# Kernel optimization log

Measured on AMD Instinct MI355X. Metric: run time of the kernel, lower is better.

Reference implementation:

```python
import jax, jax.numpy as jnp
import numpy as np

NEG_SLOPE = 0.01  # torch F.leaky_relu default
N_USER = 100000
N_ITEM = 100000
N_EDGE = 640000
D = 128
N_LAYERS = 3  # 1 input + num_hidden_layers(1) + 1 output layer


def setup_inputs() -> dict:
    key = jax.random.key(0)
    ks = jax.random.split(key, 10)
    scale = 1.0 / np.sqrt(D)
    return {
        "h_user": jax.random.normal(ks[0], (N_USER, D), dtype=jnp.float32),
        "h_item": jax.random.normal(ks[1], (N_ITEM, D), dtype=jnp.float32),
        # W[layer, etype] : etype 0 = user-follows->user, 1 = user-clicks->item, 2 = item-clicked_by->user
        "W": jax.random.normal(ks[2], (N_LAYERS, 3, D, D), dtype=jnp.float32) * scale,
        "b": jnp.zeros((N_LAYERS, 3, D), dtype=jnp.float32),
        "follows_src": jax.random.randint(ks[3], (N_EDGE,), 0, N_USER, dtype=jnp.int32),
        "follows_dst": jax.random.randint(ks[4], (N_EDGE,), 0, N_USER, dtype=jnp.int32),
        "clicks_src": jax.random.randint(ks[5], (N_EDGE,), 0, N_USER, dtype=jnp.int32),
        "clicks_dst": jax.random.randint(ks[6], (N_EDGE,), 0, N_ITEM, dtype=jnp.int32),
        "cb_src": jax.random.randint(ks[7], (N_EDGE,), 0, N_ITEM, dtype=jnp.int32),
        "cb_dst": jax.random.randint(ks[8], (N_EDGE,), 0, N_USER, dtype=jnp.int32),
    }


def _etype_conv(h_src, W, b, src, dst, n_dst):
    """Per-etype Linear on src nodes, copy_u gather, mean-aggregate at dst."""
    Wh = h_src @ W + b                     # [N_src, D] dense transform (once per node)
    msg = Wh[src]                          # [E, D] gather
    s = jax.ops.segment_sum(msg, dst, num_segments=n_dst)
    cnt = jax.ops.segment_sum(jnp.ones((src.shape[0],), dtype=Wh.dtype), dst, num_segments=n_dst)
    return s / jnp.maximum(cnt, 1.0)[:, None]  # mean; isolated nodes -> 0


def _rgcn_forward(h_user, h_item, W, b, follows_src, follows_dst,
                  clicks_src, clicks_dst, cb_src, cb_dst):
    hu, hi = h_user, h_item
    for l in range(N_LAYERS):
        # per-etype mean aggregation, then cross-etype 'sum' (DGL multi_update_all)
        agg_u = (_etype_conv(hu, W[l, 0], b[l, 0], follows_src, follows_dst, N_USER)
                 + _etype_conv(hi, W[l, 2], b[l, 2], cb_src, cb_dst, N_USER))
        agg_i = _etype_conv(hu, W[l, 1], b[l, 1], clicks_src, clicks_dst, N_ITEM)
        hu = jax.nn.leaky_relu(agg_u, NEG_SLOPE)
        hi = jax.nn.leaky_relu(agg_i, NEG_SLOPE)
    return jnp.stack([hu, hi])  # [2, 100000, 128]


def reference(h_user, h_item, W, b, follows_src, follows_dst,
              clicks_src, clicks_dst, cb_src, cb_dst):
    return _rgcn_forward(h_user, h_item, W, b, follows_src, follows_dst,
                         clicks_src, clicks_dst, cb_src, cb_dst)
```

## Files before the change

### kernel.cpp

```cpp
#include <hip/hip_runtime.h>

typedef unsigned short u16;
typedef _Float16 f16;
typedef __attribute__((ext_vector_type(8))) _Float16 f16x8;
typedef __attribute__((ext_vector_type(4))) float f32x4;

#define D 128

__global__ __launch_bounds__(256) void k_convert(const float* __restrict__ in,
                                                 u16* __restrict__ out, int n8) {
  int i = blockIdx.x * 256 + threadIdx.x;
  if (i >= n8) return;
  const float4* ip = (const float4*)in;
  float4 a = ip[i * 2], b = ip[i * 2 + 1];
  f16x8 v = {(f16)a.x, (f16)a.y, (f16)a.z, (f16)a.w,
             (f16)b.x, (f16)b.y, (f16)b.z, (f16)b.w};
  *(f16x8*)(out + (size_t)i * 8) = v;
}

__global__ __launch_bounds__(256) void k_convW(const float* __restrict__ W,
                                               u16* __restrict__ Wt, int total) {
  int idx = blockIdx.x * 256 + threadIdx.x;
  if (idx >= total) return;
  int mat = idx >> 14;
  int k = (idx >> 7) & 127;
  int n = idx & 127;
  f16 v = (f16)W[idx];
  ((f16*)Wt)[(size_t)mat * 16384 + n * 128 + k] = v;
}

__global__ __launch_bounds__(256) void k_countpos(
    const int* __restrict__ fd, const int* __restrict__ cd,
    const int* __restrict__ cbd, int* __restrict__ cnt, u16* __restrict__ pos,
    int NU, int NI, int nf, int nc, int ncb, int S) {
  int e = blockIdx.x * 256 + threadIdx.x;
  int d;
  if (e < nf)
    d = fd[e];
  else if (e < nf + nc)
    d = NU + cd[e - nf];
  else if (e < nf + nc + ncb)
    d = NU + NI + cbd[e - nf - nc];
  else
    return;
  int p = atomicAdd(&cnt[d * S], 1);
  pos[e] = (u16)p;
}

__global__ __launch_bounds__(256) void k_scanA(const int* __restrict__ cnt,
                                               int* __restrict__ part, int n, int S) {
  int t = threadIdx.x;
  int idx = blockIdx.x * 1024 + t * 4;
  int s = 0;
#pragma unroll
  for (int j = 0; j < 4; ++j)
    if (idx + j < n) s += cnt[(idx + j) * S];
  for (int off = 1; off < 64; off <<= 1) s += __shfl_down(s, off, 64);
  __shared__ int ws[4];
  if ((t & 63) == 0) ws[t >> 6] = s;
  __syncthreads();
  if (t == 0) part[blockIdx.x] = ws[0] + ws[1] + ws[2] + ws[3];
}

__global__ __launch_bounds__(1024) void k_scanB(int* __restrict__ part, int n_part) {
  __shared__ int sh[1024];
  int t = threadIdx.x;
  int v = (t < n_part) ? part[t] : 0;
  sh[t] = v;
  __syncthreads();
  for (int off = 1; off < 1024; off <<= 1) {
    int u = (t >= off) ? sh[t - off] : 0;
    __syncthreads();
    sh[t] += u;
    __syncthreads();
  }
  if (t < n_part) part[t] = sh[t] - v;
}

__global__ __launch_bounds__(256) void k_scanC(const int* __restrict__ cnt,
                                               const int* __restrict__ part,
                                               int* __restrict__ rs,
                                               int n, int total, int S) {
  int t = threadIdx.x;
  int idx = blockIdx.x * 1024 + t * 4;
  int v0 = 0, v1 = 0, v2 = 0, v3 = 0;
  if (idx < n) v0 = cnt[idx * S];
  if (idx + 1 < n) v1 = cnt[(idx + 1) * S];
  if (idx + 2 < n) v2 = cnt[(idx + 2) * S];
  if (idx + 3 < n) v3 = cnt[(idx + 3) * S];
  int s = v0 + v1 + v2 + v3;
  int inc = s;
  int lane = t & 63, w = t >> 6;
  for (int off = 1; off < 64; off <<= 1) {
    int u = __shfl_up(inc, off, 64);
    if (lane >= off) inc += u;
  }
  __shared__ int ws[4];
  if (lane == 63) ws[w] = inc;
  __syncthreads();
  int woff = 0;
  for (int i = 0; i < w; ++i) woff += ws[i];
  int ex = part[blockIdx.x] + woff + inc - s;
  int4 r;
  r.x = ex;
  r.y = ex + v0;
  r.z = r.y + v1;
  r.w = r.z + v2;
  if (idx + 3 < n)
    *(int4*)(rs + idx) = r;
  else {
    if (idx < n) rs[idx] = r.x;
    if (idx + 1 < n) rs[idx + 1] = r.y;
    if (idx + 2 < n) rs[idx + 2] = r.z;
    if (idx + 3 < n) rs[idx + 3] = r.w;
  }
  if (blockIdx.x == 0 && t == 0) rs[n] = total;
}

__global__ __launch_bounds__(256) void k_fillpos(
    const int* __restrict__ fs, const int* __restrict__ fd,
    const int* __restrict__ cs, const int* __restrict__ cd,
    const int* __restrict__ cbs, const int* __restrict__ cbd,
    const int* __restrict__ rs, const u16* __restrict__ pos,
    int* __restrict__ csr, int NU, int NI, int nf, int nc, int ncb) {
  int e = blockIdx.x * 256 + threadIdx.x;
  int d, s;
  if (e < nf) {
    d = fd[e];
    s = fs[e];
  } else if (e < nf + nc) {
    d = NU + cd[e - nf];
    s = cs[e - nf];
  } else if (e < nf + nc + ncb) {
    d = NU + NI + cbd[e - nf - nc];
    s = cbs[e - nf - nc] + NU;
  } else
    return;
  csr[rs[d] + (int)pos[e]] = s;
}

__global__ __launch_bounds__(256) void k_agg3(
    const u16* __restrict__ h_all, const int* __restrict__ csr,
    const int* __restrict__ rs, u16* __restrict__ M_all, int N3) {
  int wave = (blockIdx.x * 256 + threadIdx.x) >> 6;
  int lane = threadIdx.x & 63;
  int l16 = lane & 15;
  int w = wave * 4 + (lane >> 4);
  bool valid = w < N3;
  int wc = valid ? w : 0;
  int e = rs[wc];
  int en = valid ? rs[wc + 1] : 0;
  int deg = en - e;
  f16x8 acc0 = {0, 0, 0, 0, 0, 0, 0, 0};
  f16x8 acc1 = {0, 0, 0, 0, 0, 0, 0, 0};
  const char* hb = (const char*)h_all;
  unsigned loff = (unsigned)l16 * 16u;

  while (__any(e < en)) {
    bool a0 = e < en, a1 = e + 1 < en, a2 = e + 2 < en, a3 = e + 3 < en;
    int s0 = a0 ? csr[e] : 0;
    int s1 = a1 ? csr[e + 1] : 0;
    int s2 = a2 ? csr[e + 2] : 0;
    int s3 = a3 ? csr[e + 3] : 0;
    f16x8 v0 = {0, 0, 0, 0, 0, 0, 0, 0}, v1 = {0, 0, 0, 0, 0, 0, 0, 0};
    f16x8 v2 = {0, 0, 0, 0, 0, 0, 0, 0}, v3 = {0, 0, 0, 0, 0, 0, 0, 0};
    if (a0) v0 = *(const f16x8*)(hb + ((unsigned)s0 * 256u + loff));
    if (a1) v1 = *(const f16x8*)(hb + ((unsigned)s1 * 256u + loff));
    if (a2) v2 = *(const f16x8*)(hb + ((unsigned)s2 * 256u + loff));
    if (a3) v3 = *(const f16x8*)(hb + ((unsigned)s3 * 256u + loff));
    acc0 += v0;
    acc1 += v1;
    acc0 += v2;
    acc1 += v3;
    e += 4;
  }

  if (valid) {
    float invf = deg > 0 ? 1.0f / (float)deg : 0.f;
    f16 hinv = (f16)invf;
    f16x8 t = acc0 + acc1;
    f16x8 r = t * hinv;
    *(f16x8*)((char*)M_all + ((unsigned)wc * 256u + loff)) = r;
  }
}

template <int NE, int OUTF32>
__device__ __forceinline__ void gemm_body(
    const u16* __restrict__ mA, const u16* __restrict__ mBp,
    const u16* __restrict__ wtA, const u16* __restrict__ wtB,
    const float* __restrict__ bA, const float* __restrict__ bB,
    const int* __restrict__ rsA, const int* __restrict__ rsB,
    u16* __restrict__ o16, float* __restrict__ o32, int M, int blk) {
  int tid = threadIdx.x, lane = tid & 63, w = tid >> 6;
  int lr = lane & 15;
  int lk = (lane >> 4) * 8;
  long row0 = (long)blk * 128 + w * 32;

  f32x4 acc[2][8];
#pragma unroll
  for (int rt = 0; rt < 2; rt++)
#pragma unroll
    for (int n = 0; n < 8; n++) acc[rt][n] = (f32x4){0.f, 0.f, 0.f, 0.f};

#pragma unroll
  for (int e = 0; e < NE; ++e) {
    const f16* mm = (const f16*)((e == 0) ? mA : mBp);
    const f16* Wg = (const f16*)((e == 0) ? wtA : wtB);
#pragma unroll
    for (int ks = 0; ks < 4; ++ks) {
      int k0 = ks * 32 + lk;
      f16x8 bf[8];
#pragma unroll
      for (int n = 0; n < 8; n++) bf[n] = *(const f16x8*)(Wg + (n * 16 + lr) * D + k0);
#pragma unroll
      for (int rt = 0; rt < 2; rt++) {
        long r = row0 + rt * 16 + lr;
        if (r >= M) r = M - 1;
        f16x8 af = *(const f16x8*)(mm + r * D + k0);
#pragma unroll
        for (int n = 0; n < 8; n++)
          acc[rt][n] = __builtin_amdgcn_mfma_f32_16x16x32_f16(af, bf[n], acc[rt][n], 0, 0, 0);
      }
    }
  }

  float bAr[8], bBr[8];
#pragma unroll
  for (int n = 0; n < 8; n++) {
    bAr[n] = bA[n * 16 + lr];
    bBr[n] = (NE == 2) ? bB[n * 16 + lr] : 0.f;
  }

#pragma unroll
  for (int rt = 0; rt < 2; rt++) {
    long rbase = row0 + rt * 16 + (lane >> 4) * 4;
#pragma unroll
    for (int i = 0; i < 4; i++) {
      long r = rbase + i;
      if (r < M) {
        bool mAok = rsA[r + 1] > rsA[r];
        bool mBok = (NE == 2) && (rsB[r + 1] > rsB[r]);
#pragma unroll
        for (int n = 0; n < 8; n++) {
          int col = n * 16 + lr;
          float v = acc[rt][n][i];
          if (mAok) v += bAr[n];
          if (mBok) v += bBr[n];
          v = v > 0.f ? v : 0.01f * v;
          if (OUTF32)
            o32[r * D + col] = v;
          else
            ((f16*)o16)[r * D + col] = (f16)v;
        }
      }
    }
  }
}

template <int OUTF32>
__global__ __launch_bounds__(256) void k_gemm2(
    const u16* __restrict__ M_all, const u16* __restrict__ Wl,
    const float* __restrict__ bl, const int* __restrict__ rs_all,
    u16* __restrict__ h_all, float* __restrict__ out,
    int NU, int NI, int nbI) {
  if ((int)blockIdx.x < nbI) {
    gemm_body<1, OUTF32>(M_all + (size_t)NU * D, nullptr,
                         Wl + 16384, nullptr,
                         bl + D, nullptr,
                         rs_all + NU, nullptr,
                         h_all + (size_t)NU * D, out + (size_t)NU * D, NI,
                         blockIdx.x);
  } else {
    gemm_body<2, OUTF32>(M_all, M_all + (size_t)(NU + NI) * D,
                         Wl, Wl + 2 * 16384,
                         bl, bl + 2 * D,
                         rs_all, rs_all + NU + NI,
                         h_all, out, NU, blockIdx.x - nbI);
  }
}

extern "C" void kernel_launch(void* const* d_in, const int* in_sizes, int n_in,
                              void* d_out, int out_size, void* d_ws, size_t ws_size,
                              hipStream_t stream) {
  const float* h_user = (const float*)d_in[0];
  const float* h_item = (const float*)d_in[1];
  const float* W = (const float*)d_in[2];
  const float* bb = (const float*)d_in[3];
  const int* f_src = (const int*)d_in[4];
  const int* f_dst = (const int*)d_in[5];
  const int* c_src = (const int*)d_in[6];
  const int* c_dst = (const int*)d_in[7];
  const int* cb_src = (const int*)d_in[8];
  const int* cb_dst = (const int*)d_in[9];

  const int NU = in_sizes[0] / D;
  const int NI = in_sizes[1] / D;
  const int nEf = in_sizes[4], nEc = in_sizes[6], nEcb = in_sizes[8];
  const int N3 = NU + NI + NU;
  const int nE = nEf + nEc + nEcb;

  size_t fixed = (size_t)(N3 + 1) * 4 + 1024 * 4 + (size_t)9 * 16384 * 2 +
                 (size_t)nE * 4 + (size_t)nE * 2 +
                 (size_t)(NU + NI) * D * 2 + (size_t)N3 * D * 2 + 4096;
  int S = (fixed + (size_t)N3 * 64 <= ws_size) ? 16 : 1;

  char* p = (char*)d_ws;
  auto alloc = [&](size_t bytes) {
    char* r = p;
    p += (bytes + 255) & ~(size_t)255;
    return r;
  };
  int* cnt_pad = (int*)alloc((size_t)N3 * 4 * S);
  int* rs_all = (int*)alloc((size_t)(N3 + 1) * 4);
  int* part = (int*)alloc(1024 * 4);
  u16* Wtg = (u16*)alloc((size_t)9 * 16384 * 2);
  int* csr_all = (int*)alloc((size_t)nE * 4);
  u16* pos = (u16*)alloc((size_t)nE * 2);
  u16* h_all = (u16*)alloc((size_t)(NU + NI) * D * 2);
  u16* M_all = (u16*)alloc((size_t)N3 * D * 2);

  hipMemsetAsync(cnt_pad, 0, (size_t)N3 * 4 * S, stream);

  k_convert<<<(NU * D / 8 + 255) / 256, 256, 0, stream>>>(h_user, h_all, NU * D / 8);
  k_convert<<<(NI * D / 8 + 255) / 256, 256, 0, stream>>>(h_item, h_all + (size_t)NU * D,
                                                          NI * D / 8);
  k_convW<<<(9 * 16384 + 255) / 256, 256, 0, stream>>>(W, Wtg, 9 * 16384);

  k_countpos<<<(nE + 255) / 256, 256, 0, stream>>>(f_dst, c_dst, cb_dst, cnt_pad, pos,
                                                   NU, NI, nEf, nEc, nEcb, S);

  int n_part = (N3 + 1023) / 1024;
  k_scanA<<<n_part, 256, 0, stream>>>(cnt_pad, part, N3, S);
  k_scanB<<<1, 1024, 0, stream>>>(part, n_part);
  k_scanC<<<n_part, 256, 0, stream>>>(cnt_pad, part, rs_all, N3, nE, S);

  k_fillpos<<<(nE + 255) / 256, 256, 0, stream>>>(f_src, f_dst, c_src, c_dst,
                                                  cb_src, cb_dst, rs_all, pos,
                                                  csr_all, NU, NI, nEf, nEc, nEcb);

  int nbI = (NI + 127) / 128;
  int nbU = (NU + 127) / 128;
  int agg_blocks = ((N3 + 3) / 4 + 3) / 4;

  for (int l = 0; l < 3; ++l) {
    const u16* Wl = Wtg + (size_t)l * 3 * 16384;
    const float* bl = bb + (size_t)l * 3 * D;

    k_agg3<<<agg_blocks, 256, 0, stream>>>(h_all, csr_all, rs_all, M_all, N3);

    if (l < 2)
      k_gemm2<0><<<nbI + nbU, 256, 0, stream>>>(M_all, Wl, bl, rs_all, h_all,
                                                (float*)d_out, NU, NI, nbI);
    else
      k_gemm2<1><<<nbI + nbU, 256, 0, stream>>>(M_all, Wl, bl, rs_all, h_all,
                                                (float*)d_out, NU, NI, nbI);
  }
}
```

Baseline: 577.7 us.

## Fuse neighbor aggregation into per-layer GEMM via LDS and merge preprocessing kernels

```diff
diff --git a/kernel.cpp b/kernel.cpp
--- a/kernel.cpp
+++ b/kernel.cpp
@@ -6,45 +6,50 @@
 typedef __attribute__((ext_vector_type(4))) float f32x4;
 
 #define D 128
-
-__global__ __launch_bounds__(256) void k_convert(const float* __restrict__ in,
-                                                 u16* __restrict__ out, int n8) {
-  int i = blockIdx.x * 256 + threadIdx.x;
-  if (i >= n8) return;
-  const float4* ip = (const float4*)in;
-  float4 a = ip[i * 2], b = ip[i * 2 + 1];
-  f16x8 v = {(f16)a.x, (f16)a.y, (f16)a.z, (f16)a.w,
-             (f16)b.x, (f16)b.y, (f16)b.z, (f16)b.w};
-  *(f16x8*)(out + (size_t)i * 8) = v;
-}
-
-__global__ __launch_bounds__(256) void k_convW(const float* __restrict__ W,
-                                               u16* __restrict__ Wt, int total) {
-  int idx = blockIdx.x * 256 + threadIdx.x;
-  if (idx >= total) return;
-  int mat = idx >> 14;
-  int k = (idx >> 7) & 127;
-  int n = idx & 127;
-  f16 v = (f16)W[idx];
-  ((f16*)Wt)[(size_t)mat * 16384 + n * 128 + k] = v;
-}
-
-__global__ __launch_bounds__(256) void k_countpos(
+#define LDW 136
+
+__global__ __launch_bounds__(256) void k_pre(
+    const float* __restrict__ h_user, const float* __restrict__ h_item,
+    const float* __restrict__ W,
     const int* __restrict__ fd, const int* __restrict__ cd,
-    const int* __restrict__ cbd, int* __restrict__ cnt, u16* __restrict__ pos,
-    int NU, int NI, int nf, int nc, int ncb, int S) {
-  int e = blockIdx.x * 256 + threadIdx.x;
-  int d;
-  if (e < nf)
-    d = fd[e];
-  else if (e < nf + nc)
-    d = NU + cd[e - nf];
-  else if (e < nf + nc + ncb)
-    d = NU + NI + cbd[e - nf - nc];
-  else
-    return;
-  int p = atomicAdd(&cnt[d * S], 1);
-  pos[e] = (u16)p;
+    const int* __restrict__ cbd,
+    u16* __restrict__ h_all, u16* __restrict__ Wtg,
+    int* __restrict__ cnt, u16* __restrict__ pos,
+    int NU, int NI, int nf, int nc, int ncb, int S,
+    int nbCnt, int nbCvtU, int nbCvtI) {
+  int b = blockIdx.x;
+  if (b < nbCnt) {
+    int e = b * 256 + threadIdx.x;
+    int d;
+    if (e < nf)
+      d = fd[e];
+    else if (e < nf + nc)
+      d = NU + cd[e - nf];
+    else if (e < nf + nc + ncb)
+      d = NU + NI + cbd[e - nf - nc];
+    else
+      return;
+    int p = atomicAdd(&cnt[d * S], 1);
+    pos[e] = (u16)p;
+  } else if (b < nbCnt + nbCvtU + nbCvtI) {
+    bool isU = b < nbCnt + nbCvtU;
+    int i = (b - (isU ? nbCnt : nbCnt + nbCvtU)) * 256 + threadIdx.x;
+    int n8 = (isU ? NU : NI) * 16;
+    if (i >= n8) return;
+    const float4* ip = (const float4*)(isU ? h_user : h_item);
+    u16* op = h_all + (isU ? 0 : (size_t)NU * D);
+    float4 a = ip[i * 2], c = ip[i * 2 + 1];
+    f16x8 v = {(f16)a.x, (f16)a.y, (f16)a.z, (f16)a.w,
+               (f16)c.x, (f16)c.y, (f16)c.z, (f16)c.w};
+    *(f16x8*)(op + (size_t)i * 8) = v;
+  } else {
+    int idx = (b - nbCnt - nbCvtU - nbCvtI) * 256 + threadIdx.x;
+    if (idx >= 9 * 16384) return;
+    int mat = idx >> 14;
+    int k = (idx >> 7) & 127;
+    int n = idx & 127;
+    ((f16*)Wtg)[(size_t)mat * 16384 + n * 128 + k] = (f16)W[idx];
+  }
 }
 
 __global__ __launch_bounds__(256) void k_scanA(const int* __restrict__ cnt,
@@ -139,143 +144,136 @@
   csr[rs[d] + (int)pos[e]] = s;
 }
 
-__global__ __launch_bounds__(256) void k_agg3(
-    const u16* __restrict__ h_all, const int* __restrict__ csr,
-    const int* __restrict__ rs, u16* __restrict__ M_all, int N3) {
-  int wave = (blockIdx.x * 256 + threadIdx.x) >> 6;
+__device__ __forceinline__ void gather_wave(
+    f16 (*A)[LDW], const u16* __restrict__ h_all, const int* __restrict__ csr,
+    const int* __restrict__ rs, int gbase, int rows) {
   int lane = threadIdx.x & 63;
-  int l16 = lane & 15;
-  int w = wave * 4 + (lane >> 4);
-  bool valid = w < N3;
-  int wc = valid ? w : 0;
-  int e = rs[wc];
-  int en = valid ? rs[wc + 1] : 0;
-  int deg = en - e;
-  f16x8 acc0 = {0, 0, 0, 0, 0, 0, 0, 0};
-  f16x8 acc1 = {0, 0, 0, 0, 0, 0, 0, 0};
+  int l16 = lane & 15, grp = lane >> 4;
   const char* hb = (const char*)h_all;
   unsigned loff = (unsigned)l16 * 16u;
-
-  while (__any(e < en)) {
-    bool a0 = e < en, a1 = e + 1 < en, a2 = e + 2 < en, a3 = e + 3 < en;
-    int s0 = a0 ? csr[e] : 0;
-    int s1 = a1 ? csr[e + 1] : 0;
-    int s2 = a2 ? csr[e + 2] : 0;
-    int s3 = a3 ? csr[e + 3] : 0;
-    f16x8 v0 = {0, 0, 0, 0, 0, 0, 0, 0}, v1 = {0, 0, 0, 0, 0, 0, 0, 0};
-    f16x8 v2 = {0, 0, 0, 0, 0, 0, 0, 0}, v3 = {0, 0, 0, 0, 0, 0, 0, 0};
-    if (a0) v0 = *(const f16x8*)(hb + ((unsigned)s0 * 256u + loff));
-    if (a1) v1 = *(const f16x8*)(hb + ((unsigned)s1 * 256u + loff));
-    if (a2) v2 = *(const f16x8*)(hb + ((unsigned)s2 * 256u + loff));
-    if (a3) v3 = *(const f16x8*)(hb + ((unsigned)s3 * 256u + loff));
-    acc0 += v0;
-    acc1 += v1;
-    acc0 += v2;
-    acc1 += v3;
-    e += 4;
-  }
-
-  if (valid) {
-    float invf = deg > 0 ? 1.0f / (float)deg : 0.f;
-    f16 hinv = (f16)invf;
-    f16x8 t = acc0 + acc1;
-    f16x8 r = t * hinv;
-    *(f16x8*)((char*)M_all + ((unsigned)wc * 256u + loff)) = r;
-  }
-}
-
-template <int NE, int OUTF32>
-__device__ __forceinline__ void gemm_body(
-    const u16* __restrict__ mA, const u16* __restrict__ mBp,
-    const u16* __restrict__ wtA, const u16* __restrict__ wtB,
-    const float* __restrict__ bA, const float* __restrict__ bB,
-    const int* __restrict__ rsA, const int* __restrict__ rsB,
-    u16* __restrict__ o16, float* __restrict__ o32, int M, int blk) {
-  int tid = threadIdx.x, lane = tid & 63, w = tid >> 6;
+#pragma unroll 1
+  for (int it = 0; it < 8; ++it) {
+    int nidx = it * 4 + grp;
+    bool valid = nidx < rows;
+    int g = gbase + (valid ? nidx : 0);
+    int e = rs[g];
+    int en = valid ? rs[g + 1] : e;
+    int deg = en - e;
+    f16x8 acc0 = {0, 0, 0, 0, 0, 0, 0, 0};
+    f16x8 acc1 = {0, 0, 0, 0, 0, 0, 0, 0};
+    while (__any(e < en)) {
+      bool a0 = e < en, a1 = e + 1 < en, a2 = e + 2 < en, a3 = e + 3 < en;
+      int s0 = a0 ? csr[e] : 0;
+      int s1 = a1 ? csr[e + 1] : 0;
+      int s2 = a2 ? csr[e + 2] : 0;
+      int s3 = a3 ? csr[e + 3] : 0;
+      f16x8 v0 = {0, 0, 0, 0, 0, 0, 0, 0}, v1 = {0, 0, 0, 0, 0, 0, 0, 0};
+      f16x8 v2 = {0, 0, 0, 0, 0, 0, 0, 0}, v3 = {0, 0, 0, 0, 0, 0, 0, 0};
+      if (a0) v0 = *(const f16x8*)(hb + ((unsigned)s0 * 256u + loff));
+      if (a1) v1 = *(const f16x8*)(hb + ((unsigned)s1 * 256u + loff));
+      if (a2) v2 = *(const f16x8*)(hb + ((unsigned)s2 * 256u + loff));
+      if (a3) v3 = *(const f16x8*)(hb + ((unsigned)s3 * 256u + loff));
+      acc0 += v0;
+      acc1 += v1;
+      acc0 += v2;
+      acc1 += v3;
+      e += 4;
+    }
+    if (valid) {
+      float invf = deg > 0 ? 1.0f / (float)deg : 0.f;
+      f16 hinv = (f16)invf;
+      f16x8 t = acc0 + acc1;
+      f16x8 r = t * hinv;
+      *(f16x8*)&A[nidx][l16 * 8] = r;
+    }
+  }
+}
+
+__device__ __forceinline__ void mfma_lds(f32x4 acc[2][8], const f16 (*A)[LDW],
+                                         const u16* __restrict__ Wmat) {
+  int lane = threadIdx.x & 63;
+  int lr = lane & 15, lk = (lane >> 4) * 8;
+  const f16* Wg = (const f16*)Wmat;
+#pragma unroll
+  for (int ks = 0; ks < 4; ++ks) {
+    int k0 = ks * 32 + lk;
+    f16x8 bf[8];
+#pragma unroll
+    for (int n = 0; n < 8; ++n)
+      bf[n] = *(const f16x8*)(Wg + (n * 16 + lr) * D + k0);
+#pragma unroll
+    for (int rt = 0; rt < 2; ++rt) {
+      f16x8 af = *(const f16x8*)&A[rt * 16 + lr][k0];
+#pragma unroll
+      for (int n = 0; n < 8; ++n)
+        acc[rt][n] = __builtin_amdgcn_mfma_f32_16x16x32_f16(af, bf[n], acc[rt][n], 0, 0, 0);
+    }
+  }
+}
+
+template <int OUTF32>
+__global__ __launch_bounds__(256, 4) void k_layer(
+    const u16* __restrict__ hcur, const int* __restrict__ csr,
+    const int* __restrict__ rs_all, const u16* __restrict__ Wl,
+    const float* __restrict__ bl, u16* __restrict__ hnxt,
+    float* __restrict__ out, int NU, int NI, int nbI) {
+  __shared__ __align__(16) f16 Ash[4][32][LDW];
+  int tid = threadIdx.x, wv = tid >> 6, lane = tid & 63;
   int lr = lane & 15;
-  int lk = (lane >> 4) * 8;
-  long row0 = (long)blk * 128 + w * 32;
 
   f32x4 acc[2][8];
 #pragma unroll
-  for (int rt = 0; rt < 2; rt++)
-#pragma unroll
-    for (int n = 0; n < 8; n++) acc[rt][n] = (f32x4){0.f, 0.f, 0.f, 0.f};
-
-#pragma unroll
-  for (int e = 0; e < NE; ++e) {
-    const f16* mm = (const f16*)((e == 0) ? mA : mBp);
-    const f16* Wg = (const f16*)((e == 0) ? wtA : wtB);
-#pragma unroll
-    for (int ks = 0; ks < 4; ++ks) {
-      int k0 = ks * 32 + lk;
-      f16x8 bf[8];
-#pragma unroll
-      for (int n = 0; n < 8; n++) bf[n] = *(const f16x8*)(Wg + (n * 16 + lr) * D + k0);
-#pragma unroll
-      for (int rt = 0; rt < 2; rt++) {
-        long r = row0 + rt * 16 + lr;
-        if (r >= M) r = M - 1;
-        f16x8 af = *(const f16x8*)(mm + r * D + k0);
-#pragma unroll
-        for (int n = 0; n < 8; n++)
-          acc[rt][n] = __builtin_amdgcn_mfma_f32_16x16x32_f16(af, bf[n], acc[rt][n], 0, 0, 0);
-      }
-    }
-  }
-
+  for (int rt = 0; rt < 2; ++rt)
+#pragma unroll
+    for (int n = 0; n < 8; ++n) acc[rt][n] = (f32x4){0.f, 0.f, 0.f, 0.f};
+
+  bool isItem = (int)blockIdx.x < nbI;
+  int m0 = (isItem ? blockIdx.x : blockIdx.x - nbI) * 128;
+  int Mr = isItem ? min(128, NI - m0) : min(128, NU - m0);
+  int rows = Mr - wv * 32;
+  int gA = (isItem ? NU + m0 : m0);
+  const u16* WA = isItem ? Wl + 16384 : Wl;
+  const float* bA = isItem ? bl + D : bl;
+
+  gather_wave(Ash[wv], hcur, csr, rs_all, gA + wv * 32, rows);
+  mfma_lds(acc, Ash[wv], WA);
+  if (!isItem) {
+    gather_wave(Ash[wv], hcur, csr, rs_all, NU + NI + m0 + wv * 32, rows);
+    mfma_lds(acc, Ash[wv], Wl + 2 * 16384);
+  }
+
+  int gout = isItem ? NU + m0 : m0;
+  const int* rsA = rs_all + gA;
+  const int* rsB = rs_all + NU + NI + m0;
   float bAr[8], bBr[8];
 #pragma unroll
-  for (int n = 0; n < 8; n++) {
+  for (int n = 0; n < 8; ++n) {
     bAr[n] = bA[n * 16 + lr];
-    bBr[n] = (NE == 2) ? bB[n * 16 + lr] : 0.f;
-  }
-
-#pragma unroll
-  for (int rt = 0; rt < 2; rt++) {
-    long rbase = row0 + rt * 16 + (lane >> 4) * 4;
-#pragma unroll
-    for (int i = 0; i < 4; i++) {
-      long r = rbase + i;
-      if (r < M) {
+    bBr[n] = isItem ? 0.f : bl[2 * D + n * 16 + lr];
+  }
+#pragma unroll
+  for (int rt = 0; rt < 2; ++rt) {
+    int rbase = wv * 32 + rt * 16 + (lane >> 4) * 4;
+#pragma unroll
+    for (int i = 0; i < 4; ++i) {
+      int r = rbase + i;
+      if (r < Mr) {
         bool mAok = rsA[r + 1] > rsA[r];
-        bool mBok = (NE == 2) && (rsB[r + 1] > rsB[r]);
-#pragma unroll
-        for (int n = 0; n < 8; n++) {
+        bool mBok = (!isItem) && rsB[r + 1] > rsB[r];
+#pragma unroll
+        for (int n = 0; n < 8; ++n) {
           int col = n * 16 + lr;
           float v = acc[rt][n][i];
           if (mAok) v += bAr[n];
           if (mBok) v += bBr[n];
           v = v > 0.f ? v : 0.01f * v;
           if (OUTF32)
-            o32[r * D + col] = v;
+            out[(size_t)(gout + r) * D + col] = v;
           else
-            ((f16*)o16)[r * D + col] = (f16)v;
+            ((f16*)hnxt)[(size_t)(gout + r) * D + col] = (f16)v;
         }
       }
     }
-  }
-}
-
-template <int OUTF32>
-__global__ __launch_bounds__(256) void k_gemm2(
-    const u16* __restrict__ M_all, const u16* __restrict__ Wl,
-    const float* __restrict__ bl, const int* __restrict__ rs_all,
-    u16* __restrict__ h_all, float* __restrict__ out,
-    int NU, int NI, int nbI) {
-  if ((int)blockIdx.x < nbI) {
-    gemm_body<1, OUTF32>(M_all + (size_t)NU * D, nullptr,
-                         Wl + 16384, nullptr,
-                         bl + D, nullptr,
-                         rs_all + NU, nullptr,
-                         h_all + (size_t)NU * D, out + (size_t)NU * D, NI,
-                         blockIdx.x);
-  } else {
-    gemm_body<2, OUTF32>(M_all, M_all + (size_t)(NU + NI) * D,
-                         Wl, Wl + 2 * 16384,
-                         bl, bl + 2 * D,
-                         rs_all, rs_all + NU + NI,
-                         h_all, out, NU, blockIdx.x - nbI);
   }
 }
 
@@ -301,8 +299,8 @@
 
   size_t fixed = (size_t)(N3 + 1) * 4 + 1024 * 4 + (size_t)9 * 16384 * 2 +
                  (size_t)nE * 4 + (size_t)nE * 2 +
-                 (size_t)(NU + NI) * D * 2 + (size_t)N3 * D * 2 + 4096;
-  int S = (fixed + (size_t)N3 * 64 <= ws_size) ? 16 : 1;
+                 2 * (size_t)(NU + NI) * D * 2 + (size_t)N3 * 4 + 8192;
+  int S = (fixed + (size_t)N3 * 60 <= ws_size) ? 16 : 1;
 
   char* p = (char*)d_ws;
   auto alloc = [&](size_t bytes) {
@@ -316,18 +314,18 @@
   u16* Wtg = (u16*)alloc((size_t)9 * 16384 * 2);
   int* csr_all = (int*)alloc((size_t)nE * 4);
   u16* pos = (u16*)alloc((size_t)nE * 2);
-  u16* h_all = (u16*)alloc((size_t)(NU + NI) * D * 2);
-  u16* M_all = (u16*)alloc((size_t)N3 * D * 2);
+  u16* hA = (u16*)alloc((size_t)(NU + NI) * D * 2);
+  u16* hB = (u16*)alloc((size_t)(NU + NI) * D * 2);
 
   hipMemsetAsync(cnt_pad, 0, (size_t)N3 * 4 * S, stream);
 
-  k_convert<<<(NU * D / 8 + 255) / 256, 256, 0, stream>>>(h_user, h_all, NU * D / 8);
-  k_convert<<<(NI * D / 8 + 255) / 256, 256, 0, stream>>>(h_item, h_all + (size_t)NU * D,
-                                                          NI * D / 8);
-  k_convW<<<(9 * 16384 + 255) / 256, 256, 0, stream>>>(W, Wtg, 9 * 16384);
-
-  k_countpos<<<(nE + 255) / 256, 256, 0, stream>>>(f_dst, c_dst, cb_dst, cnt_pad, pos,
-                                                   NU, NI, nEf, nEc, nEcb, S);
+  int nbCnt = (nE + 255) / 256;
+  int nbCvtU = (NU * 16 + 255) / 256;
+  int nbCvtI = (NI * 16 + 255) / 256;
+  int nbW = (9 * 16384 + 255) / 256;
+  k_pre<<<nbCnt + nbCvtU + nbCvtI + nbW, 256, 0, stream>>>(
+      h_user, h_item, W, f_dst, c_dst, cb_dst, hA, Wtg, cnt_pad, pos,
+      NU, NI, nEf, nEc, nEcb, S, nbCnt, nbCvtU, nbCvtI);
 
   int n_part = (N3 + 1023) / 1024;
   k_scanA<<<n_part, 256, 0, stream>>>(cnt_pad, part, N3, S);
@@ -340,19 +338,20 @@
 
   int nbI = (NI + 127) / 128;
   int nbU = (NU + 127) / 128;
-  int agg_blocks = ((N3 + 3) / 4 + 3) / 4;
-
+
+  u16* hcur = hA;
+  u16* hnxt = hB;
   for (int l = 0; l < 3; ++l) {
     const u16* Wl = Wtg + (size_t)l * 3 * 16384;
     const float* bl = bb + (size_t)l * 3 * D;
-
-    k_agg3<<<agg_blocks, 256, 0, stream>>>(h_all, csr_all, rs_all, M_all, N3);
-
     if (l < 2)
-      k_gemm2<0><<<nbI + nbU, 256, 0, stream>>>(M_all, Wl, bl, rs_all, h_all,
-                                                (float*)d_out, NU, NI, nbI);
+      k_layer<0><<<nbI + nbU, 256, 0, stream>>>(hcur, csr_all, rs_all, Wl, bl,
+                                                hnxt, (float*)d_out, NU, NI, nbI);
     else
-      k_gemm2<1><<<nbI + nbU, 256, 0, stream>>>(M_all, Wl, bl, rs_all, h_all,
-                                                (float*)d_out, NU, NI, nbI);
-  }
-}
+      k_layer<1><<<nbI + nbU, 256, 0, stream>>>(hcur, csr_all, rs_all, Wl, bl,
+                                                hnxt, (float*)d_out, NU, NI, nbI);
+    u16* t = hcur;
+    hcur = hnxt;
+    hnxt = t;
+  }
+}
```

Result: slower. 707.6 us (+22.5%).
